# Optimization experiments

Measured on AMD Instinct MI355X. Metric: run time of the kernel, lower is better.

Reference implementation:

```python
import jax, jax.numpy as jnp
import numpy as np

S, B, F, H, K = 256, 2048, 5, 64, 8  # seq, batch, feat, hidden, num aux inputs


def setup_inputs() -> dict:
    key = jax.random.key(0)
    ks = jax.random.split(key, 20)
    def rn(k, shape, s=1.0):
        return jax.random.normal(k, shape, dtype=jnp.float32) * s
    inp = {}
    names = ["Y"] + ["x%d" % i for i in range(1, 9)]
    for i, nm in enumerate(names):
        inp[nm] = rn(ks[i], (S, B, F))
    p = 0.1  # weight scale for stability
    inp["W_main"] = rn(ks[9], (F, 4 * H), p)   # main-input proj for gates [i,f,o,c]
    inp["U_main"] = rn(ks[10], (H, 4 * H), p)
    inp["b_main"] = jnp.zeros((4 * H,), jnp.float32)
    inp["W_aux"] = rn(ks[11], (K, F, 2 * H), p)  # per-aux proj for [i_k, c_k]
    inp["U_aux"] = rn(ks[12], (K, H, 2 * H), p)
    inp["b_aux"] = jnp.zeros((K, 2 * H), jnp.float32)
    inp["W_att"] = rn(ks[13], (H, H), p)        # attention bilinear form vs C_{t-1}
    inp["b_att"] = jnp.zeros((1,), jnp.float32)
    inp["W_ih"] = rn(ks[14], (4 * H, H), p)     # standard LSTM (torch gate order i,f,g,o)
    inp["W_hh"] = rn(ks[15], (4 * H, H), p)
    inp["b_ih"] = jnp.zeros((4 * H,), jnp.float32)
    inp["b_hh"] = jnp.zeros((4 * H,), jnp.float32)
    inp["lin_W"] = rn(ks[16], (1, H), p)
    inp["lin_b"] = jnp.zeros((1,), jnp.float32)
    return inp


def _forward(Y, x1, x2, x3, x4, x5, x6, x7, x8,
             W_main, U_main, b_main, W_aux, U_aux, b_aux, W_att, b_att,
             W_ih, W_hh, b_ih, b_hh, lin_W, lin_b):
    Hd = U_main.shape[0]
    X = jnp.stack([x1, x2, x3, x4, x5, x6, x7, x8], axis=2)  # (S,B,K,F)
    Bsz = Y.shape[1]
    h0 = jnp.zeros((Bsz, Hd), Y.dtype)
    c0 = jnp.zeros((Bsz, Hd), Y.dtype)

    def mi_step(carry, t):
        h, c = carry
        yt, xt = t  # (B,F), (B,K,F)
        gm = yt @ W_main + h @ U_main + b_main  # (B,4H)
        i = jax.nn.sigmoid(gm[:, :Hd])
        f = jax.nn.sigmoid(gm[:, Hd:2 * Hd])
        o = jax.nn.sigmoid(gm[:, 2 * Hd:3 * Hd])
        cm = jnp.tanh(gm[:, 3 * Hd:])
        ga = (jnp.einsum('bkf,kfg->bkg', xt, W_aux)
              + jnp.einsum('bh,khg->bkg', h, U_aux) + b_aux)  # (B,K,2H)
        ik = jax.nn.sigmoid(ga[..., :Hd])
        ck = jnp.tanh(ga[..., Hd:])
        # candidate contributions: main + each auxiliary -> (B,K+1,H)
        l = jnp.concatenate([(i * cm)[:, None, :], ik * ck], axis=1)
        # attention of each candidate against previous cell state
        u = jnp.tanh(jnp.einsum('bkh,hg,bg->bk', l, W_att, c) + b_att)  # (B,K+1)
        a = jax.nn.softmax(u, axis=-1)
        L = jnp.einsum('bk,bkh->bh', a, l)
        c_new = f * c + L
        h_new = o * jnp.tanh(c_new)
        return (h_new, c_new), h_new

    _, hs = jax.lax.scan(mi_step, (h0, c0), (Y, X))  # hs: (S,B,H)

    # standard LSTM over the MI-LSTM hidden sequence
    pre = hs @ W_ih.T + (b_ih + b_hh)  # (S,B,4H)

    def lstm_step(carry, g_in):
        h, c = carry
        g = g_in + h @ W_hh.T
        i = jax.nn.sigmoid(g[:, :Hd])
        f = jax.nn.sigmoid(g[:, Hd:2 * Hd])
        gg = jnp.tanh(g[:, 2 * Hd:3 * Hd])
        o = jax.nn.sigmoid(g[:, 3 * Hd:])
        c = f * c + i * gg
        h = o * jnp.tanh(c)
        return (h, c), h

    _, outs = jax.lax.scan(lstm_step, (h0, c0), pre)  # (S,B,H)
    return jax.nn.relu(outs) @ lin_W.T + lin_b  # (S,B,1)


def reference(Y, x1, x2, x3, x4, x5, x6, x7, x8,
              W_main, U_main, b_main, W_aux, U_aux, b_aux, W_att, b_att,
              W_ih, W_hh, b_ih, b_hh, lin_W, lin_b):
    return _forward(Y, x1, x2, x3, x4, x5, x6, x7, x8,
                    W_main, U_main, b_main, W_aux, U_aux, b_aux, W_att, b_att,
                    W_ih, W_hh, b_ih, b_hh, lin_W, lin_b)
```

## Files before the change

### kernel.cpp

```cpp
#include <hip/hip_runtime.h>
#include <cstddef>
#include <math.h>

#define SEQ   256
#define BATCH 2048
#define FD    5
#define HD    64
#define NCOL  1280
#define ROWS  8
#define NTHR  512

__device__ __forceinline__ float sigm(float x) { return 1.0f / (1.0f + expf(-x)); }
__device__ __forceinline__ float tanh_f(float x) { return tanhf(x); }

__device__ __forceinline__ float wave_sum(float v) {
#pragma unroll
    for (int m = 1; m < 64; m <<= 1) v += __shfl_xor(v, m);
    return v;
}

__global__ void transpose_u(const float* __restrict__ U_main,
                            const float* __restrict__ U_aux,
                            float* __restrict__ Ut) {
    const int c = blockIdx.x;
    const int h = threadIdx.x;
    float v;
    if (c < 256) {
        v = U_main[h * 256 + c];
    } else {
        int cp = c - 256, kk = cp >> 7, gg = cp & 127;
        v = U_aux[(size_t)kk * 64 * 128 + h * 128 + gg];
    }
    Ut[c * 64 + h] = v;
}

__global__ __launch_bounds__(NTHR, 1)
void minet_fused(const float* __restrict__ Y,
                 const float* __restrict__ x1, const float* __restrict__ x2,
                 const float* __restrict__ x3, const float* __restrict__ x4,
                 const float* __restrict__ x5, const float* __restrict__ x6,
                 const float* __restrict__ x7, const float* __restrict__ x8,
                 const float* __restrict__ W_main, const float* __restrict__ Ut,
                 const float* __restrict__ b_main, const float* __restrict__ W_aux,
                 const float* __restrict__ b_aux,
                 const float* __restrict__ W_att,  const float* __restrict__ b_att,
                 const float* __restrict__ W_ih,   const float* __restrict__ W_hh,
                 const float* __restrict__ b_ih,   const float* __restrict__ b_hh,
                 const float* __restrict__ lin_W,  const float* __restrict__ lin_b,
                 float* __restrict__ out)
{
    __shared__ __align__(16) float h1[ROWS][HD];
    __shared__ __align__(16) float c1[ROWS][HD];
    __shared__ __align__(16) float h2[ROWS][HD];
    __shared__ __align__(16) float outb[ROWS][NCOL];
    __shared__ __align__(16) float outg[2][ROWS][256];
    __shared__ __align__(16) float inb[ROWS][9][8];
    __shared__ __align__(16) float WaT[HD * HD];

    const int tid  = threadIdx.x;
    const int lane = tid & 63;
    const int wid  = tid >> 6;
    const int b0   = blockIdx.x * ROWS;
    const bool has3 = (tid < 256);

    for (int i = tid; i < HD * HD; i += NTHR) {
        int g = i >> 6, h = i & 63;
        WaT[i] = W_att[h * 64 + g];
    }

    int colv[3];
    colv[0] = tid; colv[1] = tid + 512; colv[2] = has3 ? tid + 1024 : 0;
    float wf[3][5];
    float bias[3];
    int   inoff[3];
    const float* utp[3];
#pragma unroll
    for (int j = 0; j < 3; ++j) {
        if (j < 2 || has3) {
            int c = colv[j];
            utp[j] = Ut + (size_t)c * 64;
            if (c < 256) {
#pragma unroll
                for (int f = 0; f < FD; ++f) wf[j][f] = W_main[f * 256 + c];
                bias[j]  = b_main[c];
                inoff[j] = 0;
            } else {
                int cp = c - 256, kk = cp >> 7, gg = cp & 127;
#pragma unroll
                for (int f = 0; f < FD; ++f) wf[j][f] = W_aux[(kk * 5 + f) * 128 + gg];
                bias[j]  = b_aux[kk * 128 + gg];
                inoff[j] = (1 + kk) * 8;
            }
        } else {
            utp[j] = Ut; bias[j] = 0.0f; inoff[j] = 0;
#pragma unroll
            for (int f = 0; f < FD; ++f) wf[j][f] = 0.0f;
        }
    }

    const int  cc      = tid & 255;
    const bool ispart1 = (tid >= 256);
    const float* wcol  = (ispart1 ? W_hh : W_ih) + (size_t)cc * 64;
    const float  b2    = ispart1 ? 0.0f : (b_ih[cc] + b_hh[cc]);

    const float linw = lin_W[lane];
    const float linb = lin_b[0];
    const float batt = b_att[0];

    for (int i = tid; i < ROWS * HD; i += NTHR) {
        (&h1[0][0])[i] = 0.0f; (&c1[0][0])[i] = 0.0f; (&h2[0][0])[i] = 0.0f;
    }
    for (int i = tid; i < ROWS * 9 * 8; i += NTHR) (&inb[0][0][0])[i] = 0.0f;
    float c2 = 0.0f;

    const bool pon = (tid < 360);
    const float* psrc = Y;
    int pofs = 0;
    float pf = 0.0f;
    if (pon) {
        int r = tid / 45, rem = tid % 45;
        int s = rem / 5, f = rem % 5;
        const float* base = Y;
        if (s == 1) base = x1; else if (s == 2) base = x2; else if (s == 3) base = x3;
        else if (s == 4) base = x4; else if (s == 5) base = x5; else if (s == 6) base = x6;
        else if (s == 7) base = x7; else if (s == 8) base = x8;
        psrc = base + (size_t)(b0 + r) * FD + f;
        pofs = (r * 9 + s) * 8 + f;
        pf   = psrc[0];
    }

    for (int t = 0; t < SEQ; ++t) {
        if (pon) (&inb[0][0][0])[pofs] = pf;
        __syncthreads();

        if (pon && t + 1 < SEQ) pf = psrc[(size_t)(t + 1) * BATCH * FD];

        float acc[3][ROWS];
#pragma unroll
        for (int j = 0; j < 3; ++j) {
            if (j < 2 || has3) {
#pragma unroll
                for (int r = 0; r < ROWS; ++r) {
                    const float* ip = &inb[r][0][0] + inoff[j];
                    float4 ia = *(const float4*)ip;
                    float  i4 = ip[4];
                    acc[j][r] = bias[j] + ia.x * wf[j][0] + ia.y * wf[j][1] + ia.z * wf[j][2]
                                        + ia.w * wf[j][3] + i4 * wf[j][4];
                }
            }
        }
#pragma unroll 2
        for (int hb = 0; hb < 16; ++hb) {
            float4 w0 = *(const float4*)(utp[0] + hb * 4);
            float4 w1 = *(const float4*)(utp[1] + hb * 4);
            float4 w2 = has3 ? *(const float4*)(utp[2] + hb * 4) : w0;
#pragma unroll
            for (int r = 0; r < ROWS; ++r) {
                float4 h4 = *(const float4*)&h1[r][hb * 4];
                acc[0][r] = fmaf(h4.x, w0.x, fmaf(h4.y, w0.y,
                            fmaf(h4.z, w0.z, fmaf(h4.w, w0.w, acc[0][r]))));
                acc[1][r] = fmaf(h4.x, w1.x, fmaf(h4.y, w1.y,
                            fmaf(h4.z, w1.z, fmaf(h4.w, w1.w, acc[1][r]))));
                if (has3)
                    acc[2][r] = fmaf(h4.x, w2.x, fmaf(h4.y, w2.y,
                                fmaf(h4.z, w2.z, fmaf(h4.w, w2.w, acc[2][r]))));
            }
        }
#pragma unroll
        for (int j = 0; j < 3; ++j) {
            if (j < 2 || has3) {
#pragma unroll
                for (int r = 0; r < ROWS; ++r)
                    outb[r][colv[j]] = acc[j][r];
            }
        }

        float v0 = 0.0f;
        {
            float cr0 = c1[wid][lane];
#pragma unroll
            for (int g = 0; g < 64; ++g) {
                float w = WaT[g * 64 + lane];
                v0 = fmaf(__shfl(cr0, g), w, v0);
            }
        }
        __syncthreads();

        {
            const int r = wid;
            float gi = outb[r][lane],       gf = outb[r][64 + lane];
            float go = outb[r][128 + lane], gc = outb[r][192 + lane];
            float ii = sigm(gi), ff = sigm(gf), oo = sigm(go), cm = tanh_f(gc);
            float l[9];
            l[0] = ii * cm;
#pragma unroll
            for (int k = 1; k <= 8; ++k) {
                float a_ = outb[r][256 + (k - 1) * 128 + lane];
                float b_ = outb[r][256 + (k - 1) * 128 + 64 + lane];
                l[k] = sigm(a_) * tanh_f(b_);
            }
            float u[9]; float umax = -1e30f;
#pragma unroll
            for (int k = 0; k < 9; ++k) {
                float p = wave_sum(l[k] * v0);
                u[k] = tanh_f(p + batt);
                umax = fmaxf(umax, u[k]);
            }
            float den = 0.0f, Lh = 0.0f;
#pragma unroll
            for (int k = 0; k < 9; ++k) {
                float e = expf(u[k] - umax);
                den += e;
                Lh = fmaf(e, l[k], Lh);
            }
            Lh /= den;
            float cp = c1[r][lane];
            float cn = fmaf(ff, cp, Lh);
            float hn = oo * tanh_f(cn);
            c1[r][lane] = cn;
            h1[r][lane] = hn;
        }
        __syncthreads();

        {
            float accg[ROWS];
#pragma unroll
            for (int r = 0; r < ROWS; ++r) accg[r] = b2;
            const float(*SS)[HD] = ispart1 ? h2 : h1;
#pragma unroll 4
            for (int hb = 0; hb < 16; ++hb) {
                float4 w4 = *(const float4*)(wcol + hb * 4);
#pragma unroll
                for (int r = 0; r < ROWS; ++r) {
                    float4 s4 = *(const float4*)&SS[r][hb * 4];
                    accg[r] = fmaf(s4.x, w4.x, fmaf(s4.y, w4.y,
                              fmaf(s4.z, w4.z, fmaf(s4.w, w4.w, accg[r]))));
                }
            }
#pragma unroll
            for (int r = 0; r < ROWS; ++r)
                outg[ispart1 ? 1 : 0][r][cc] = accg[r];
        }
        __syncthreads();

        {
            const int r = wid;
            float g0 = outg[0][r][lane]       + outg[1][r][lane];
            float g1 = outg[0][r][64 + lane]  + outg[1][r][64 + lane];
            float g2 = outg[0][r][128 + lane] + outg[1][r][128 + lane];
            float g3 = outg[0][r][192 + lane] + outg[1][r][192 + lane];
            float i2 = sigm(g0), f2 = sigm(g1), gg = tanh_f(g2), o2 = sigm(g3);
            float cn = fmaf(f2, c2, i2 * gg);
            c2 = cn;
            float hn = o2 * tanh_f(cn);
            h2[r][lane] = hn;
            float e = wave_sum(fmaxf(hn, 0.0f) * linw);
            if (lane == 0) out[(size_t)t * BATCH + b0 + r] = e + linb;
        }
    }
}

extern "C" void kernel_launch(void* const* d_in, const int* in_sizes, int n_in,
                              void* d_out, int out_size, void* d_ws, size_t ws_size,
                              hipStream_t stream) {
    const float* Y      = (const float*)d_in[0];
    const float* x1     = (const float*)d_in[1];
    const float* x2     = (const float*)d_in[2];
    const float* x3     = (const float*)d_in[3];
    const float* x4     = (const float*)d_in[4];
    const float* x5     = (const float*)d_in[5];
    const float* x6     = (const float*)d_in[6];
    const float* x7     = (const float*)d_in[7];
    const float* x8     = (const float*)d_in[8];
    const float* W_main = (const float*)d_in[9];
    const float* U_main = (const float*)d_in[10];
    const float* b_main = (const float*)d_in[11];
    const float* W_aux  = (const float*)d_in[12];
    const float* U_aux  = (const float*)d_in[13];
    const float* b_aux  = (const float*)d_in[14];
    const float* W_att  = (const float*)d_in[15];
    const float* b_att  = (const float*)d_in[16];
    const float* W_ih   = (const float*)d_in[17];
    const float* W_hh   = (const float*)d_in[18];
    const float* b_ih   = (const float*)d_in[19];
    const float* b_hh   = (const float*)d_in[20];
    const float* lin_W  = (const float*)d_in[21];
    const float* lin_b  = (const float*)d_in[22];
    float* out = (float*)d_out;
    float* Ut  = (float*)d_ws;

    transpose_u<<<dim3(NCOL), dim3(HD), 0, stream>>>(U_main, U_aux, Ut);

    dim3 grid(BATCH / ROWS);
    dim3 block(NTHR);
    minet_fused<<<grid, block, 0, stream>>>(Y, x1, x2, x3, x4, x5, x6, x7, x8,
                                            W_main, Ut, b_main, W_aux, b_aux,
                                            W_att, b_att, W_ih, W_hh, b_ih, b_hh,
                                            lin_W, lin_b, out);
}
```

Baseline: 7.573 ms.

## Halve rows per block and fold attention projection into recurrent matvec

Each block now processes 4 batch rows with 256 threads instead of 8 rows with 512 threads, so the grid doubles to 512 blocks and launch bounds allow two blocks per CU. Each thread computes five gate columns instead of two or three, and the second LSTM's matvec does two columns per thread. The W_att·c projection moves out of a per-wave shuffle loop with a shared WaT copy into the main recurrent matvec: it is appended as extra transposed columns in the workspace and computed by the first wave. This aims to improve occupancy and latency hiding on the sequential recurrence, at the cost of more registers per thread and load imbalance where only one wave handles the attention columns.

```diff
diff --git a/kernel.cpp b/kernel.cpp
--- a/kernel.cpp
+++ b/kernel.cpp
@@ -7,8 +7,10 @@
 #define FD    5
 #define HD    64
 #define NCOL  1280
-#define ROWS  8
-#define NTHR  512
+#define NCOLE 1344
+#define ROWS  4
+#define NTHR  256
+#define NBLK  (BATCH / ROWS)
 
 __device__ __forceinline__ float sigm(float x) { return 1.0f / (1.0f + expf(-x)); }
 __device__ __forceinline__ float tanh_f(float x) { return tanhf(x); }
@@ -21,29 +23,31 @@
 
 __global__ void transpose_u(const float* __restrict__ U_main,
                             const float* __restrict__ U_aux,
-                            float* __restrict__ Ut) {
+                            const float* __restrict__ W_att,
+                            float* __restrict__ UtE) {
     const int c = blockIdx.x;
     const int h = threadIdx.x;
     float v;
     if (c < 256) {
         v = U_main[h * 256 + c];
-    } else {
+    } else if (c < 1280) {
         int cp = c - 256, kk = cp >> 7, gg = cp & 127;
         v = U_aux[(size_t)kk * 64 * 128 + h * 128 + gg];
-    }
-    Ut[c * 64 + h] = v;
+    } else {
+        v = W_att[(c - 1280) * 64 + h];
+    }
+    UtE[c * 64 + h] = v;
 }
 
-__global__ __launch_bounds__(NTHR, 1)
+__global__ __launch_bounds__(NTHR, 2)
 void minet_fused(const float* __restrict__ Y,
                  const float* __restrict__ x1, const float* __restrict__ x2,
                  const float* __restrict__ x3, const float* __restrict__ x4,
                  const float* __restrict__ x5, const float* __restrict__ x6,
                  const float* __restrict__ x7, const float* __restrict__ x8,
-                 const float* __restrict__ W_main, const float* __restrict__ Ut,
+                 const float* __restrict__ W_main, const float* __restrict__ UtE,
                  const float* __restrict__ b_main, const float* __restrict__ W_aux,
-                 const float* __restrict__ b_aux,
-                 const float* __restrict__ W_att,  const float* __restrict__ b_att,
+                 const float* __restrict__ b_aux,  const float* __restrict__ b_att,
                  const float* __restrict__ W_ih,   const float* __restrict__ W_hh,
                  const float* __restrict__ b_ih,   const float* __restrict__ b_hh,
                  const float* __restrict__ lin_W,  const float* __restrict__ lin_b,
@@ -52,56 +56,47 @@
     __shared__ __align__(16) float h1[ROWS][HD];
     __shared__ __align__(16) float c1[ROWS][HD];
     __shared__ __align__(16) float h2[ROWS][HD];
-    __shared__ __align__(16) float outb[ROWS][NCOL];
+    __shared__ __align__(16) float outb[ROWS][NCOLE];
     __shared__ __align__(16) float outg[2][ROWS][256];
     __shared__ __align__(16) float inb[ROWS][9][8];
-    __shared__ __align__(16) float WaT[HD * HD];
 
     const int tid  = threadIdx.x;
     const int lane = tid & 63;
     const int wid  = tid >> 6;
     const int b0   = blockIdx.x * ROWS;
-    const bool has3 = (tid < 256);
-
-    for (int i = tid; i < HD * HD; i += NTHR) {
-        int g = i >> 6, h = i & 63;
-        WaT[i] = W_att[h * 64 + g];
-    }
-
-    int colv[3];
-    colv[0] = tid; colv[1] = tid + 512; colv[2] = has3 ? tid + 1024 : 0;
-    float wf[3][5];
-    float bias[3];
-    int   inoff[3];
-    const float* utp[3];
-#pragma unroll
-    for (int j = 0; j < 3; ++j) {
-        if (j < 2 || has3) {
-            int c = colv[j];
-            utp[j] = Ut + (size_t)c * 64;
-            if (c < 256) {
-#pragma unroll
-                for (int f = 0; f < FD; ++f) wf[j][f] = W_main[f * 256 + c];
-                bias[j]  = b_main[c];
-                inoff[j] = 0;
-            } else {
-                int cp = c - 256, kk = cp >> 7, gg = cp & 127;
-#pragma unroll
-                for (int f = 0; f < FD; ++f) wf[j][f] = W_aux[(kk * 5 + f) * 128 + gg];
-                bias[j]  = b_aux[kk * 128 + gg];
-                inoff[j] = (1 + kk) * 8;
-            }
+    const bool isw0 = (tid < 64);
+
+    float wf[5][5];
+    float bias[5];
+    int   inoff[5];
+    const float* utp[5];
+#pragma unroll
+    for (int j = 0; j < 5; ++j) {
+        const int c = tid + 256 * j;
+        utp[j] = UtE + (size_t)c * 64;
+        if (j == 0) {
+#pragma unroll
+            for (int f = 0; f < FD; ++f) wf[j][f] = W_main[f * 256 + c];
+            bias[j]  = b_main[c];
+            inoff[j] = 0;
         } else {
-            utp[j] = Ut; bias[j] = 0.0f; inoff[j] = 0;
-#pragma unroll
-            for (int f = 0; f < FD; ++f) wf[j][f] = 0.0f;
-        }
-    }
-
-    const int  cc      = tid & 255;
-    const bool ispart1 = (tid >= 256);
-    const float* wcol  = (ispart1 ? W_hh : W_ih) + (size_t)cc * 64;
-    const float  b2    = ispart1 ? 0.0f : (b_ih[cc] + b_hh[cc]);
+            int cp = c - 256, kk = cp >> 7, gg = cp & 127;
+#pragma unroll
+            for (int f = 0; f < FD; ++f) wf[j][f] = W_aux[(kk * 5 + f) * 128 + gg];
+            bias[j]  = b_aux[kk * 128 + gg];
+            inoff[j] = (1 + kk) * 8;
+        }
+    }
+    const float* uta = UtE + (size_t)(1280 + tid) * 64;
+
+    const int  cc      = tid & 127;
+    const bool ispart1 = (tid >= 128);
+    const float* wbase = ispart1 ? W_hh : W_ih;
+    const float* wcol0 = wbase + (size_t)cc * 64;
+    const float* wcol1 = wbase + (size_t)(cc + 128) * 64;
+    float b2[2];
+    b2[0] = ispart1 ? 0.0f : (b_ih[cc] + b_hh[cc]);
+    b2[1] = ispart1 ? 0.0f : (b_ih[cc + 128] + b_hh[cc + 128]);
 
     const float linw = lin_W[lane];
     const float linb = lin_b[0];
@@ -113,7 +108,7 @@
     for (int i = tid; i < ROWS * 9 * 8; i += NTHR) (&inb[0][0][0])[i] = 0.0f;
     float c2 = 0.0f;
 
-    const bool pon = (tid < 360);
+    const bool pon = (tid < 180);
     const float* psrc = Y;
     int pofs = 0;
     float pf = 0.0f;
@@ -135,25 +130,28 @@
 
         if (pon && t + 1 < SEQ) pf = psrc[(size_t)(t + 1) * BATCH * FD];
 
-        float acc[3][ROWS];
-#pragma unroll
-        for (int j = 0; j < 3; ++j) {
-            if (j < 2 || has3) {
-#pragma unroll
-                for (int r = 0; r < ROWS; ++r) {
-                    const float* ip = &inb[r][0][0] + inoff[j];
-                    float4 ia = *(const float4*)ip;
-                    float  i4 = ip[4];
-                    acc[j][r] = bias[j] + ia.x * wf[j][0] + ia.y * wf[j][1] + ia.z * wf[j][2]
-                                        + ia.w * wf[j][3] + i4 * wf[j][4];
-                }
-            }
-        }
+        float acc[5][ROWS];
+#pragma unroll
+        for (int j = 0; j < 5; ++j) {
+#pragma unroll
+            for (int r = 0; r < ROWS; ++r) {
+                const float* ip = &inb[r][0][0] + inoff[j];
+                float4 ia = *(const float4*)ip;
+                float  i4 = ip[4];
+                acc[j][r] = bias[j] + ia.x * wf[j][0] + ia.y * wf[j][1] + ia.z * wf[j][2]
+                                    + ia.w * wf[j][3] + i4 * wf[j][4];
+            }
+        }
+        float vac[ROWS] = {0.0f, 0.0f, 0.0f, 0.0f};
 #pragma unroll 2
         for (int hb = 0; hb < 16; ++hb) {
             float4 w0 = *(const float4*)(utp[0] + hb * 4);
             float4 w1 = *(const float4*)(utp[1] + hb * 4);
-            float4 w2 = has3 ? *(const float4*)(utp[2] + hb * 4) : w0;
+            float4 w2 = *(const float4*)(utp[2] + hb * 4);
+            float4 w3 = *(const float4*)(utp[3] + hb * 4);
+            float4 w4 = *(const float4*)(utp[4] + hb * 4);
+            float4 wa;
+            if (isw0) wa = *(const float4*)(uta + hb * 4);
 #pragma unroll
             for (int r = 0; r < ROWS; ++r) {
                 float4 h4 = *(const float4*)&h1[r][hb * 4];
@@ -161,33 +159,34 @@
                             fmaf(h4.z, w0.z, fmaf(h4.w, w0.w, acc[0][r]))));
                 acc[1][r] = fmaf(h4.x, w1.x, fmaf(h4.y, w1.y,
                             fmaf(h4.z, w1.z, fmaf(h4.w, w1.w, acc[1][r]))));
-                if (has3)
-                    acc[2][r] = fmaf(h4.x, w2.x, fmaf(h4.y, w2.y,
-                                fmaf(h4.z, w2.z, fmaf(h4.w, w2.w, acc[2][r]))));
-            }
-        }
-#pragma unroll
-        for (int j = 0; j < 3; ++j) {
-            if (j < 2 || has3) {
-#pragma unroll
-                for (int r = 0; r < ROWS; ++r)
-                    outb[r][colv[j]] = acc[j][r];
-            }
-        }
-
-        float v0 = 0.0f;
-        {
-            float cr0 = c1[wid][lane];
-#pragma unroll
-            for (int g = 0; g < 64; ++g) {
-                float w = WaT[g * 64 + lane];
-                v0 = fmaf(__shfl(cr0, g), w, v0);
-            }
+                acc[2][r] = fmaf(h4.x, w2.x, fmaf(h4.y, w2.y,
+                            fmaf(h4.z, w2.z, fmaf(h4.w, w2.w, acc[2][r]))));
+                acc[3][r] = fmaf(h4.x, w3.x, fmaf(h4.y, w3.y,
+                            fmaf(h4.z, w3.z, fmaf(h4.w, w3.w, acc[3][r]))));
+                acc[4][r] = fmaf(h4.x, w4.x, fmaf(h4.y, w4.y,
+                            fmaf(h4.z, w4.z, fmaf(h4.w, w4.w, acc[4][r]))));
+                if (isw0) {
+                    float4 c4 = *(const float4*)&c1[r][hb * 4];
+                    vac[r] = fmaf(c4.x, wa.x, fmaf(c4.y, wa.y,
+                             fmaf(c4.z, wa.z, fmaf(c4.w, wa.w, vac[r]))));
+                }
+            }
+        }
+#pragma unroll
+        for (int j = 0; j < 5; ++j)
+#pragma unroll
+            for (int r = 0; r < ROWS; ++r)
+                outb[r][tid + 256 * j] = acc[j][r];
+        if (isw0) {
+#pragma unroll
+            for (int r = 0; r < ROWS; ++r)
+                outb[r][1280 + tid] = vac[r];
         }
         __syncthreads();
 
         {
             const int r = wid;
+            const float v0 = outb[r][1280 + lane];
             float gi = outb[r][lane],       gf = outb[r][64 + lane];
             float go = outb[r][128 + lane], gc = outb[r][192 + lane];
             float ii = sigm(gi), ff = sigm(gf), oo = sigm(go), cm = tanh_f(gc);
@@ -223,23 +222,31 @@
         __syncthreads();
 
         {
-            float accg[ROWS];
-#pragma unroll
-            for (int r = 0; r < ROWS; ++r) accg[r] = b2;
+            float accg[2][ROWS];
+#pragma unroll
+            for (int q = 0; q < 2; ++q)
+#pragma unroll
+                for (int r = 0; r < ROWS; ++r) accg[q][r] = b2[q];
             const float(*SS)[HD] = ispart1 ? h2 : h1;
 #pragma unroll 4
             for (int hb = 0; hb < 16; ++hb) {
-                float4 w4 = *(const float4*)(wcol + hb * 4);
+                float4 wA = *(const float4*)(wcol0 + hb * 4);
+                float4 wB = *(const float4*)(wcol1 + hb * 4);
 #pragma unroll
                 for (int r = 0; r < ROWS; ++r) {
                     float4 s4 = *(const float4*)&SS[r][hb * 4];
-                    accg[r] = fmaf(s4.x, w4.x, fmaf(s4.y, w4.y,
-                              fmaf(s4.z, w4.z, fmaf(s4.w, w4.w, accg[r]))));
+                    accg[0][r] = fmaf(s4.x, wA.x, fmaf(s4.y, wA.y,
+                                 fmaf(s4.z, wA.z, fmaf(s4.w, wA.w, accg[0][r]))));
+                    accg[1][r] = fmaf(s4.x, wB.x, fmaf(s4.y, wB.y,
+                                 fmaf(s4.z, wB.z, fmaf(s4.w, wB.w, accg[1][r]))));
                 }
             }
-#pragma unroll
-            for (int r = 0; r < ROWS; ++r)
-                outg[ispart1 ? 1 : 0][r][cc] = accg[r];
+            const int part = ispart1 ? 1 : 0;
+#pragma unroll
+            for (int r = 0; r < ROWS; ++r) {
+                outg[part][r][cc]       = accg[0][r];
+                outg[part][r][cc + 128] = accg[1][r];
+            }
         }
         __syncthreads();
 
@@ -287,14 +294,14 @@
     const float* lin_W  = (const float*)d_in[21];
     const float* lin_b  = (const float*)d_in[22];
     float* out = (float*)d_out;
-    float* Ut  = (float*)d_ws;
-
-    transpose_u<<<dim3(NCOL), dim3(HD), 0, stream>>>(U_main, U_aux, Ut);
-
-    dim3 grid(BATCH / ROWS);
+    float* UtE = (float*)d_ws;
+
+    transpose_u<<<dim3(NCOLE), dim3(HD), 0, stream>>>(U_main, U_aux, W_att, UtE);
+
+    dim3 grid(NBLK);
     dim3 block(NTHR);
     minet_fused<<<grid, block, 0, stream>>>(Y, x1, x2, x3, x4, x5, x6, x7, x8,
-                                            W_main, Ut, b_main, W_aux, b_aux,
-                                            W_att, b_att, W_ih, W_hh, b_ih, b_hh,
+                                            W_main, UtE, b_main, W_aux, b_aux,
+                                            b_att, W_ih, W_hh, b_ih, b_hh,
                                             lin_W, lin_b, out);
 }
```

Measured after the change: 12.20 ms. 1.61x slower.

## Restructure recurrence so each wave owns two batch rows without block barriers

Applied to the files above, without the earlier changes.

Each wavefront now handles two batch rows end to end: every lane computes all 21 column groups (gates, aux gates and the attention vector folded in as an extra column) for its hidden index, so no block-wide __syncthreads is needed per timestep. A prep kernel interleaves U, W_att, input weights and biases into a float4-friendly layout read straight from global/L2 instead of shared memory. The intent is to remove barrier and LDS staging overhead. In exchange every wave re-reads the full weight set from cache each step, with much higher register pressure and less weight reuse per load.

```diff
diff --git a/kernel.cpp b/kernel.cpp
--- a/kernel.cpp
+++ b/kernel.cpp
@@ -6,257 +6,241 @@
 #define BATCH 2048
 #define FD    5
 #define HD    64
-#define NCOL  1280
-#define ROWS  8
-#define NTHR  512
+#define NJ    21
+#define WAVES 4
+#define NTHR  256
+#define STEP_STRIDE (BATCH * FD)
 
 __device__ __forceinline__ float sigm(float x) { return 1.0f / (1.0f + expf(-x)); }
-__device__ __forceinline__ float tanh_f(float x) { return tanhf(x); }
 
 __device__ __forceinline__ float wave_sum(float v) {
 #pragma unroll
     for (int m = 1; m < 64; m <<= 1) v += __shfl_xor(v, m);
     return v;
 }
-
-__global__ void transpose_u(const float* __restrict__ U_main,
-                            const float* __restrict__ U_aux,
-                            float* __restrict__ Ut) {
-    const int c = blockIdx.x;
-    const int h = threadIdx.x;
-    float v;
-    if (c < 256) {
-        v = U_main[h * 256 + c];
-    } else {
-        int cp = c - 256, kk = cp >> 7, gg = cp & 127;
-        v = U_aux[(size_t)kk * 64 * 128 + h * 128 + gg];
-    }
-    Ut[c * 64 + h] = v;
-}
+__device__ __forceinline__ float fma4(float4 w, float4 h, float a) {
+    return fmaf(w.x, h.x, fmaf(w.y, h.y, fmaf(w.z, h.z, fmaf(w.w, h.w, a))));
+}
+
+__global__ void prep_weights(const float* __restrict__ U_main,
+                             const float* __restrict__ U_aux,
+                             const float* __restrict__ W_att,
+                             const float* __restrict__ W_main,
+                             const float* __restrict__ W_aux,
+                             const float* __restrict__ b_main,
+                             const float* __restrict__ b_aux,
+                             float* __restrict__ ws) {
+    const int j = blockIdx.x;
+    const int lane = threadIdx.x;
+    const int col = lane + 64 * j;
+    float4* UtW = (float4*)ws;
+    float*  Wfb = ws + (size_t)16 * NJ * 64 * 4;
+    for (int hb = 0; hb < 16; ++hb) {
+        float4 w;
+        if (col < 256) {
+            w.x = U_main[(4 * hb + 0) * 256 + col];
+            w.y = U_main[(4 * hb + 1) * 256 + col];
+            w.z = U_main[(4 * hb + 2) * 256 + col];
+            w.w = U_main[(4 * hb + 3) * 256 + col];
+        } else if (col < 1280) {
+            int cp = col - 256, kk = cp >> 7, gg = cp & 127;
+            const float* ub = U_aux + (size_t)kk * 64 * 128 + gg;
+            w.x = ub[(4 * hb + 0) * 128];
+            w.y = ub[(4 * hb + 1) * 128];
+            w.z = ub[(4 * hb + 2) * 128];
+            w.w = ub[(4 * hb + 3) * 128];
+        } else {
+            w = *(const float4*)(W_att + (size_t)(col - 1280) * 64 + 4 * hb);
+        }
+        UtW[((size_t)hb * NJ + j) * 64 + lane] = w;
+    }
+    float w0 = 0, w1 = 0, w2 = 0, w3 = 0, w4 = 0, bb = 0;
+    if (col < 256) {
+        w0 = W_main[0 * 256 + col]; w1 = W_main[1 * 256 + col];
+        w2 = W_main[2 * 256 + col]; w3 = W_main[3 * 256 + col];
+        w4 = W_main[4 * 256 + col]; bb = b_main[col];
+    } else if (col < 1280) {
+        int cp = col - 256, kk = cp >> 7, gg = cp & 127;
+        w0 = W_aux[(kk * 5 + 0) * 128 + gg]; w1 = W_aux[(kk * 5 + 1) * 128 + gg];
+        w2 = W_aux[(kk * 5 + 2) * 128 + gg]; w3 = W_aux[(kk * 5 + 3) * 128 + gg];
+        w4 = W_aux[(kk * 5 + 4) * 128 + gg]; bb = b_aux[kk * 128 + gg];
+    }
+    float* d = Wfb + ((size_t)j * 64 + lane) * 8;
+    d[0] = w0; d[1] = w1; d[2] = w2; d[3] = w3; d[4] = w4; d[5] = bb; d[6] = 0; d[7] = 0;
+}
+
+#define P5_ROW(ACC, CREG, RR)                                                 \
+    {                                                                         \
+        float ii = sigm(ACC[0]), ff = sigm(ACC[1]), oo = sigm(ACC[2]);        \
+        float cm = tanhf(ACC[3]);                                             \
+        float vv = ACC[20];                                                   \
+        float l[9]; l[0] = ii * cm;                                           \
+        _Pragma("unroll")                                                     \
+        for (int k = 1; k <= 8; ++k)                                          \
+            l[k] = sigm(ACC[2 + 2 * k]) * tanhf(ACC[3 + 2 * k]);              \
+        float u[9]; float um = -1e30f;                                        \
+        _Pragma("unroll")                                                     \
+        for (int k = 0; k < 9; ++k) {                                         \
+            u[k] = tanhf(wave_sum(l[k] * vv) + batt);                         \
+            um = fmaxf(um, u[k]);                                             \
+        }                                                                     \
+        float den = 0.f, Lh = 0.f;                                            \
+        _Pragma("unroll")                                                     \
+        for (int k = 0; k < 9; ++k) {                                         \
+            float e = expf(u[k] - um); den += e; Lh = fmaf(e, l[k], Lh);      \
+        }                                                                     \
+        Lh /= den;                                                            \
+        float cn = fmaf(ff, CREG, Lh); CREG = cn;                             \
+        float hn = oo * tanhf(cn);                                            \
+        hbc[wid][RR][lane] = hn; cbc[wid][RR][lane] = cn;                     \
+    }
+
+#define P7_ROW(PRE, C2, RR)                                                   \
+    {                                                                         \
+        float i2 = sigm(PRE[0]), f2 = sigm(PRE[1]);                           \
+        float g2 = tanhf(PRE[2]), o2 = sigm(PRE[3]);                          \
+        C2 = fmaf(f2, C2, i2 * g2);                                           \
+        float hn2 = o2 * tanhf(C2);                                           \
+        h2b[wid][RR][lane] = hn2;                                             \
+        float e = wave_sum(fmaxf(hn2, 0.f) * linw);                           \
+        if (lane == 0) out[(size_t)t * BATCH + row0 + RR] = e + linb;         \
+    }
 
 __global__ __launch_bounds__(NTHR, 1)
-void minet_fused(const float* __restrict__ Y,
-                 const float* __restrict__ x1, const float* __restrict__ x2,
-                 const float* __restrict__ x3, const float* __restrict__ x4,
-                 const float* __restrict__ x5, const float* __restrict__ x6,
-                 const float* __restrict__ x7, const float* __restrict__ x8,
-                 const float* __restrict__ W_main, const float* __restrict__ Ut,
-                 const float* __restrict__ b_main, const float* __restrict__ W_aux,
-                 const float* __restrict__ b_aux,
-                 const float* __restrict__ W_att,  const float* __restrict__ b_att,
-                 const float* __restrict__ W_ih,   const float* __restrict__ W_hh,
-                 const float* __restrict__ b_ih,   const float* __restrict__ b_hh,
-                 const float* __restrict__ lin_W,  const float* __restrict__ lin_b,
-                 float* __restrict__ out)
+void minet_wave(const float* __restrict__ Y,
+                const float* __restrict__ x1, const float* __restrict__ x2,
+                const float* __restrict__ x3, const float* __restrict__ x4,
+                const float* __restrict__ x5, const float* __restrict__ x6,
+                const float* __restrict__ x7, const float* __restrict__ x8,
+                const float4* __restrict__ UtW, const float* __restrict__ Wfb,
+                const float* __restrict__ W_ih, const float* __restrict__ W_hh,
+                const float* __restrict__ b_ih, const float* __restrict__ b_hh,
+                const float* __restrict__ lin_W, const float* __restrict__ lin_b,
+                const float* __restrict__ b_att,
+                float* __restrict__ out)
 {
-    __shared__ __align__(16) float h1[ROWS][HD];
-    __shared__ __align__(16) float c1[ROWS][HD];
-    __shared__ __align__(16) float h2[ROWS][HD];
-    __shared__ __align__(16) float outb[ROWS][NCOL];
-    __shared__ __align__(16) float outg[2][ROWS][256];
-    __shared__ __align__(16) float inb[ROWS][9][8];
-    __shared__ __align__(16) float WaT[HD * HD];
+    __shared__ __align__(16) float hbc[WAVES][2][HD];
+    __shared__ __align__(16) float cbc[WAVES][2][HD];
+    __shared__ __align__(16) float h2b[WAVES][2][HD];
+    __shared__ __align__(16) float inw[WAVES][2][72];
 
     const int tid  = threadIdx.x;
     const int lane = tid & 63;
     const int wid  = tid >> 6;
-    const int b0   = blockIdx.x * ROWS;
-    const bool has3 = (tid < 256);
-
-    for (int i = tid; i < HD * HD; i += NTHR) {
-        int g = i >> 6, h = i & 63;
-        WaT[i] = W_att[h * 64 + g];
-    }
-
-    int colv[3];
-    colv[0] = tid; colv[1] = tid + 512; colv[2] = has3 ? tid + 1024 : 0;
-    float wf[3][5];
-    float bias[3];
-    int   inoff[3];
-    const float* utp[3];
-#pragma unroll
-    for (int j = 0; j < 3; ++j) {
-        if (j < 2 || has3) {
-            int c = colv[j];
-            utp[j] = Ut + (size_t)c * 64;
-            if (c < 256) {
-#pragma unroll
-                for (int f = 0; f < FD; ++f) wf[j][f] = W_main[f * 256 + c];
-                bias[j]  = b_main[c];
-                inoff[j] = 0;
-            } else {
-                int cp = c - 256, kk = cp >> 7, gg = cp & 127;
-#pragma unroll
-                for (int f = 0; f < FD; ++f) wf[j][f] = W_aux[(kk * 5 + f) * 128 + gg];
-                bias[j]  = b_aux[kk * 128 + gg];
-                inoff[j] = (1 + kk) * 8;
-            }
-        } else {
-            utp[j] = Ut; bias[j] = 0.0f; inoff[j] = 0;
-#pragma unroll
-            for (int f = 0; f < FD; ++f) wf[j][f] = 0.0f;
-        }
-    }
-
-    const int  cc      = tid & 255;
-    const bool ispart1 = (tid >= 256);
-    const float* wcol  = (ispart1 ? W_hh : W_ih) + (size_t)cc * 64;
-    const float  b2    = ispart1 ? 0.0f : (b_ih[cc] + b_hh[cc]);
-
+    const int row0 = blockIdx.x * (WAVES * 2) + wid * 2;
+
+    hbc[wid][0][lane] = 0.f; hbc[wid][1][lane] = 0.f;
+    cbc[wid][0][lane] = 0.f; cbc[wid][1][lane] = 0.f;
+    h2b[wid][0][lane] = 0.f; h2b[wid][1][lane] = 0.f;
+    inw[wid][0][lane] = 0.f; inw[wid][1][lane] = 0.f;
+    if (lane < 8) { inw[wid][0][64 + lane] = 0.f; inw[wid][1][64 + lane] = 0.f; }
+
+    float b2q[4];
+    const float* wih[4];
+    const float* whh[4];
+#pragma unroll
+    for (int q = 0; q < 4; ++q) {
+        b2q[q] = b_ih[64 * q + lane] + b_hh[64 * q + lane];
+        wih[q] = W_ih + (size_t)(64 * q + lane) * 64;
+        whh[q] = W_hh + (size_t)(64 * q + lane) * 64;
+    }
     const float linw = lin_W[lane];
     const float linb = lin_b[0];
     const float batt = b_att[0];
 
-    for (int i = tid; i < ROWS * HD; i += NTHR) {
-        (&h1[0][0])[i] = 0.0f; (&c1[0][0])[i] = 0.0f; (&h2[0][0])[i] = 0.0f;
-    }
-    for (int i = tid; i < ROWS * 9 * 8; i += NTHR) (&inb[0][0][0])[i] = 0.0f;
-    float c2 = 0.0f;
-
-    const bool pon = (tid < 360);
-    const float* psrc = Y;
-    int pofs = 0;
-    float pf = 0.0f;
-    if (pon) {
-        int r = tid / 45, rem = tid % 45;
-        int s = rem / 5, f = rem % 5;
-        const float* base = Y;
-        if (s == 1) base = x1; else if (s == 2) base = x2; else if (s == 3) base = x3;
-        else if (s == 4) base = x4; else if (s == 5) base = x5; else if (s == 6) base = x6;
-        else if (s == 7) base = x7; else if (s == 8) base = x8;
-        psrc = base + (size_t)(b0 + r) * FD + f;
-        pofs = (r * 9 + s) * 8 + f;
-        pf   = psrc[0];
-    }
+    int rA = lane / 45, remA = lane % 45, sA = remA / 5, fA = remA % 5;
+    const float* bA;
+    switch (sA) {
+        case 0: bA = Y;  break; case 1: bA = x1; break; case 2: bA = x2; break;
+        case 3: bA = x3; break; case 4: bA = x4; break; case 5: bA = x5; break;
+        case 6: bA = x6; break; case 7: bA = x7; break; default: bA = x8; break;
+    }
+    const float* psrcA = bA + (size_t)(row0 + rA) * FD + fA;
+    const int lofsA = rA * 72 + sA * 8 + fA;
+
+    const bool vB = (lane < 26);
+    int idxB = lane + 64;
+    int rB = idxB / 45, remB = idxB % 45, sB = remB / 5, fB = remB % 5;
+    const float* bB;
+    switch (sB) {
+        case 0: bB = Y;  break; case 1: bB = x1; break; case 2: bB = x2; break;
+        case 3: bB = x3; break; case 4: bB = x4; break; case 5: bB = x5; break;
+        case 6: bB = x6; break; case 7: bB = x7; break; default: bB = x8; break;
+    }
+    const float* psrcB = bB + (size_t)(row0 + rB) * FD + fB;
+    const int lofsB = rB * 72 + sB * 8 + fB;
+
+    float pfA = psrcA[0];
+    float pfB = vB ? psrcB[0] : 0.f;
+
+    float c1r0 = 0.f, c1r1 = 0.f;
+    float c2r0 = 0.f, c2r1 = 0.f;
 
     for (int t = 0; t < SEQ; ++t) {
-        if (pon) (&inb[0][0][0])[pofs] = pf;
-        __syncthreads();
-
-        if (pon && t + 1 < SEQ) pf = psrc[(size_t)(t + 1) * BATCH * FD];
-
-        float acc[3][ROWS];
-#pragma unroll
-        for (int j = 0; j < 3; ++j) {
-            if (j < 2 || has3) {
-#pragma unroll
-                for (int r = 0; r < ROWS; ++r) {
-                    const float* ip = &inb[r][0][0] + inoff[j];
-                    float4 ia = *(const float4*)ip;
-                    float  i4 = ip[4];
-                    acc[j][r] = bias[j] + ia.x * wf[j][0] + ia.y * wf[j][1] + ia.z * wf[j][2]
-                                        + ia.w * wf[j][3] + i4 * wf[j][4];
-                }
-            }
+        (&inw[wid][0][0])[lofsA] = pfA;
+        if (vB) (&inw[wid][0][0])[lofsB] = pfB;
+        if (t + 1 < SEQ) {
+            pfA = psrcA[(size_t)(t + 1) * STEP_STRIDE];
+            if (vB) pfB = psrcB[(size_t)(t + 1) * STEP_STRIDE];
+        }
+
+        float acc0[NJ], acc1[NJ];
+#pragma unroll
+        for (int j = 0; j < NJ; ++j) {
+            const float* wb = Wfb + ((size_t)j * 64 + lane) * 8;
+            float4 wf = *(const float4*)wb;
+            float  w4 = wb[4], bj = wb[5];
+            const int s = (j < 4) ? 0 : ((j < 20) ? (1 + ((j - 4) >> 1)) : 0);
+            const float* iA = &inw[wid][0][s * 8];
+            const float* iB = &inw[wid][1][s * 8];
+            float4 a4 = *(const float4*)iA; float a4e = iA[4];
+            float4 e4 = *(const float4*)iB; float e4e = iB[4];
+            acc0[j] = fmaf(a4e, w4, fma4(wf, a4, bj));
+            acc1[j] = fmaf(e4e, w4, fma4(wf, e4, bj));
         }
 #pragma unroll 2
         for (int hb = 0; hb < 16; ++hb) {
-            float4 w0 = *(const float4*)(utp[0] + hb * 4);
-            float4 w1 = *(const float4*)(utp[1] + hb * 4);
-            float4 w2 = has3 ? *(const float4*)(utp[2] + hb * 4) : w0;
-#pragma unroll
-            for (int r = 0; r < ROWS; ++r) {
-                float4 h4 = *(const float4*)&h1[r][hb * 4];
-                acc[0][r] = fmaf(h4.x, w0.x, fmaf(h4.y, w0.y,
-                            fmaf(h4.z, w0.z, fmaf(h4.w, w0.w, acc[0][r]))));
-                acc[1][r] = fmaf(h4.x, w1.x, fmaf(h4.y, w1.y,
-                            fmaf(h4.z, w1.z, fmaf(h4.w, w1.w, acc[1][r]))));
-                if (has3)
-                    acc[2][r] = fmaf(h4.x, w2.x, fmaf(h4.y, w2.y,
-                                fmaf(h4.z, w2.z, fmaf(h4.w, w2.w, acc[2][r]))));
+            float4 hA = *(const float4*)&hbc[wid][0][hb * 4];
+            float4 hB = *(const float4*)&hbc[wid][1][hb * 4];
+            float4 cA = *(const float4*)&cbc[wid][0][hb * 4];
+            float4 cB = *(const float4*)&cbc[wid][1][hb * 4];
+            const float4* wrow = UtW + ((size_t)hb * NJ) * 64 + lane;
+#pragma unroll
+            for (int j = 0; j < 20; ++j) {
+                float4 w = wrow[j * 64];
+                acc0[j] = fma4(w, hA, acc0[j]);
+                acc1[j] = fma4(w, hB, acc1[j]);
             }
-        }
-#pragma unroll
-        for (int j = 0; j < 3; ++j) {
-            if (j < 2 || has3) {
-#pragma unroll
-                for (int r = 0; r < ROWS; ++r)
-                    outb[r][colv[j]] = acc[j][r];
+            {
+                float4 w = wrow[20 * 64];
+                acc0[20] = fma4(w, cA, acc0[20]);
+                acc1[20] = fma4(w, cB, acc1[20]);
             }
         }
 
-        float v0 = 0.0f;
-        {
-            float cr0 = c1[wid][lane];
-#pragma unroll
-            for (int g = 0; g < 64; ++g) {
-                float w = WaT[g * 64 + lane];
-                v0 = fmaf(__shfl(cr0, g), w, v0);
+        P5_ROW(acc0, c1r0, 0)
+        P5_ROW(acc1, c1r1, 1)
+
+        float pre0[4], pre1[4];
+#pragma unroll
+        for (int q = 0; q < 4; ++q) { pre0[q] = b2q[q]; pre1[q] = b2q[q]; }
+#pragma unroll 4
+        for (int hb = 0; hb < 16; ++hb) {
+            float4 hA = *(const float4*)&hbc[wid][0][hb * 4];
+            float4 hB = *(const float4*)&hbc[wid][1][hb * 4];
+            float4 gA = *(const float4*)&h2b[wid][0][hb * 4];
+            float4 gB = *(const float4*)&h2b[wid][1][hb * 4];
+#pragma unroll
+            for (int q = 0; q < 4; ++q) {
+                float4 wi = *(const float4*)(wih[q] + hb * 4);
+                float4 wh = *(const float4*)(whh[q] + hb * 4);
+                pre0[q] = fma4(wh, gA, fma4(wi, hA, pre0[q]));
+                pre1[q] = fma4(wh, gB, fma4(wi, hB, pre1[q]));
             }
         }
-        __syncthreads();
-
-        {
-            const int r = wid;
-            float gi = outb[r][lane],       gf = outb[r][64 + lane];
-            float go = outb[r][128 + lane], gc = outb[r][192 + lane];
-            float ii = sigm(gi), ff = sigm(gf), oo = sigm(go), cm = tanh_f(gc);
-            float l[9];
-            l[0] = ii * cm;
-#pragma unroll
-            for (int k = 1; k <= 8; ++k) {
-                float a_ = outb[r][256 + (k - 1) * 128 + lane];
-                float b_ = outb[r][256 + (k - 1) * 128 + 64 + lane];
-                l[k] = sigm(a_) * tanh_f(b_);
-            }
-            float u[9]; float umax = -1e30f;
-#pragma unroll
-            for (int k = 0; k < 9; ++k) {
-                float p = wave_sum(l[k] * v0);
-                u[k] = tanh_f(p + batt);
-                umax = fmaxf(umax, u[k]);
-            }
-            float den = 0.0f, Lh = 0.0f;
-#pragma unroll
-            for (int k = 0; k < 9; ++k) {
-                float e = expf(u[k] - umax);
-                den += e;
-                Lh = fmaf(e, l[k], Lh);
-            }
-            Lh /= den;
-            float cp = c1[r][lane];
-            float cn = fmaf(ff, cp, Lh);
-            float hn = oo * tanh_f(cn);
-            c1[r][lane] = cn;
-            h1[r][lane] = hn;
-        }
-        __syncthreads();
-
-        {
-            float accg[ROWS];
-#pragma unroll
-            for (int r = 0; r < ROWS; ++r) accg[r] = b2;
-            const float(*SS)[HD] = ispart1 ? h2 : h1;
-#pragma unroll 4
-            for (int hb = 0; hb < 16; ++hb) {
-                float4 w4 = *(const float4*)(wcol + hb * 4);
-#pragma unroll
-                for (int r = 0; r < ROWS; ++r) {
-                    float4 s4 = *(const float4*)&SS[r][hb * 4];
-                    accg[r] = fmaf(s4.x, w4.x, fmaf(s4.y, w4.y,
-                              fmaf(s4.z, w4.z, fmaf(s4.w, w4.w, accg[r]))));
-                }
-            }
-#pragma unroll
-            for (int r = 0; r < ROWS; ++r)
-                outg[ispart1 ? 1 : 0][r][cc] = accg[r];
-        }
-        __syncthreads();
-
-        {
-            const int r = wid;
-            float g0 = outg[0][r][lane]       + outg[1][r][lane];
-            float g1 = outg[0][r][64 + lane]  + outg[1][r][64 + lane];
-            float g2 = outg[0][r][128 + lane] + outg[1][r][128 + lane];
-            float g3 = outg[0][r][192 + lane] + outg[1][r][192 + lane];
-            float i2 = sigm(g0), f2 = sigm(g1), gg = tanh_f(g2), o2 = sigm(g3);
-            float cn = fmaf(f2, c2, i2 * gg);
-            c2 = cn;
-            float hn = o2 * tanh_f(cn);
-            h2[r][lane] = hn;
-            float e = wave_sum(fmaxf(hn, 0.0f) * linw);
-            if (lane == 0) out[(size_t)t * BATCH + b0 + r] = e + linb;
-        }
+
+        P7_ROW(pre0, c2r0, 0)
+        P7_ROW(pre1, c2r1, 1)
     }
 }
 
@@ -287,14 +271,17 @@
     const float* lin_W  = (const float*)d_in[21];
     const float* lin_b  = (const float*)d_in[22];
     float* out = (float*)d_out;
-    float* Ut  = (float*)d_ws;
-
-    transpose_u<<<dim3(NCOL), dim3(HD), 0, stream>>>(U_main, U_aux, Ut);
-
-    dim3 grid(BATCH / ROWS);
+    float* ws  = (float*)d_ws;
+
+    prep_weights<<<dim3(NJ), dim3(HD), 0, stream>>>(U_main, U_aux, W_att,
+                                                    W_main, W_aux, b_main, b_aux, ws);
+
+    const float4* UtW = (const float4*)ws;
+    const float*  Wfb = ws + (size_t)16 * NJ * 64 * 4;
+
+    dim3 grid(BATCH / (WAVES * 2));
     dim3 block(NTHR);
-    minet_fused<<<grid, block, 0, stream>>>(Y, x1, x2, x3, x4, x5, x6, x7, x8,
-                                            W_main, Ut, b_main, W_aux, b_aux,
-                                            W_att, b_att, W_ih, W_hh, b_ih, b_hh,
-                                            lin_W, lin_b, out);
-}
+    minet_wave<<<grid, block, 0, stream>>>(Y, x1, x2, x3, x4, x5, x6, x7, x8,
+                                           UtW, Wfb, W_ih, W_hh, b_ih, b_hh,
+                                           lin_W, lin_b, b_att, out);
+}
```

New measurement: 12.24 ms. +61.6%, slower.
